# Kernel tuning notes

Hardware: AMD Instinct MI355X
Metric: run time of the kernel (lower is better)

Reference implementation:

```python
import jax, jax.numpy as jnp
import numpy as np

NUM_SRC1, NUM_DST1 = 2_000_000, 131_072
NUM_SRC2, NUM_DST2 = 131_072, 8_192
E1, E2 = NUM_DST1 * 15, NUM_DST2 * 15
F_IN, F_H = 128, 128


def setup_inputs() -> dict:
    key = jax.random.key(0)
    ks = jax.random.split(key, 10)
    return {
        "x": jax.random.normal(ks[0], (NUM_SRC1, F_IN), dtype=jnp.float32),
        "edge1_src": jax.random.randint(ks[1], (E1,), 0, NUM_SRC1, dtype=jnp.int32),
        "edge1_dst": jax.random.randint(ks[2], (E1,), 0, NUM_DST1, dtype=jnp.int32),
        "edge2_src": jax.random.randint(ks[3], (E2,), 0, NUM_SRC2, dtype=jnp.int32),
        "edge2_dst": jax.random.randint(ks[4], (E2,), 0, NUM_DST2, dtype=jnp.int32),
        "num_dst1": NUM_DST1,
        "num_dst2": NUM_DST2,
        "W_self1": jax.random.normal(ks[5], (F_IN, F_H), dtype=jnp.float32) * 0.05,
        "W_neigh1": jax.random.normal(ks[6], (F_IN, F_H), dtype=jnp.float32) * 0.05,
        "b1": jnp.zeros((F_H,), dtype=jnp.float32),
        "W_self2": jax.random.normal(ks[7], (F_H, F_H), dtype=jnp.float32) * 0.05,
        "W_neigh2": jax.random.normal(ks[8], (F_H, F_H), dtype=jnp.float32) * 0.05,
        "b2": jnp.zeros((F_H,), dtype=jnp.float32),
    }


def _sage_mean(h_src, h_dst, e_src, e_dst, num_dst, W_self, W_neigh, b):
    # mean-aggregate neighbor feats per dst, then linear transforms (DGL SAGEConv, aggr='mean')
    agg = jax.ops.segment_sum(h_src[e_src], e_dst, num_segments=num_dst)  # [num_dst, F]
    deg = jax.ops.segment_sum(jnp.ones((e_dst.shape[0],), h_src.dtype), e_dst,
                              num_segments=num_dst)
    mean = agg / jnp.maximum(deg, 1.0)[:, None]
    return h_dst @ W_self + mean @ W_neigh + b


def reference(x, edge1_src, edge1_dst, edge2_src, edge2_dst, num_dst1, num_dst2,
              W_self1, W_neigh1, b1, W_self2, W_neigh2, b2):
    h_dst = x[:num_dst1]
    h = _sage_mean(x, h_dst, edge1_src, edge1_dst, num_dst1, W_self1, W_neigh1, b1)
    h = jax.nn.relu(h)
    h_dst2 = h[:num_dst2]
    out = _sage_mean(h, h_dst2, edge2_src, edge2_dst, num_dst2, W_self2, W_neigh2, b2)
    return out
```

## Files before the change

kernel.cpp:

```cpp
#include <hip/hip_runtime.h>

static constexpr int FDIM = 128;
static constexpr int ND1  = 131072;
static constexpr int ND2  = 8192;
static constexpr int PADW = 64;
static constexpr int LDP  = 56;

using bf16x8 = __attribute__((ext_vector_type(8))) short;
using u16x8  = __attribute__((ext_vector_type(8))) unsigned short;
using f32x4  = __attribute__((ext_vector_type(4))) float;

static __device__ __forceinline__ unsigned short f2bf(float f) {
  unsigned u = __float_as_uint(f);
  u = (u + 0x7FFFu + ((u >> 16) & 1u)) >> 16;
  return (unsigned short)u;
}
static __device__ __forceinline__ float bf2f(unsigned short s) {
  return __uint_as_float(((unsigned)s) << 16);
}

__global__ void build_pad(const int* __restrict__ e1s, const int* __restrict__ e1d,
                          const int* __restrict__ e2s, const int* __restrict__ e2d,
                          int* __restrict__ cnt1, int* __restrict__ cnt2,
                          int* __restrict__ pad1, int* __restrict__ pad2,
                          int E1, int E2, int nb_fill,
                          const float* __restrict__ Ws1, const float* __restrict__ Wn1,
                          unsigned short* __restrict__ Wt1,
                          const float* __restrict__ Ws2, const float* __restrict__ Wn2,
                          unsigned short* __restrict__ Wt2) {
  if ((int)blockIdx.x >= nb_fill) {
    int t = (blockIdx.x - nb_fill) * 256 + threadIdx.x;
    int which = t >> 15;
    int r = t & 32767;
    int col = r >> 8, k = r & 255;
    const float* Ws = which ? Ws2 : Ws1;
    const float* Wn = which ? Wn2 : Wn1;
    unsigned short* Wt = which ? Wt2 : Wt1;
    float v = (k < 128) ? Ws[k * 128 + col] : Wn[(k - 128) * 128 + col];
    Wt[col * 256 + k] = f2bf(v);
    return;
  }
  const int n1 = E1 >> 2, n2 = E2 >> 2;
  int t = blockIdx.x * 256 + threadIdx.x;
  if (t < n1) {
    int4 d = ((const int4*)e1d)[t];
    int4 s = ((const int4*)e1s)[t];
    int p;
    p = atomicAdd(&cnt1[d.x], 1); if (p < PADW) pad1[d.x * PADW + p] = s.x;
    p = atomicAdd(&cnt1[d.y], 1); if (p < PADW) pad1[d.y * PADW + p] = s.y;
    p = atomicAdd(&cnt1[d.z], 1); if (p < PADW) pad1[d.z * PADW + p] = s.z;
    p = atomicAdd(&cnt1[d.w], 1); if (p < PADW) pad1[d.w * PADW + p] = s.w;
  } else if (t < n1 + n2) {
    int4 d = ((const int4*)e2d)[t - n1];
    int4 s = ((const int4*)e2s)[t - n1];
    int p;
    p = atomicAdd(&cnt2[d.x], 1); if (p < PADW) pad2[d.x * PADW + p] = s.x;
    p = atomicAdd(&cnt2[d.y], 1); if (p < PADW) pad2[d.y * PADW + p] = s.y;
    p = atomicAdd(&cnt2[d.z], 1); if (p < PADW) pad2[d.z * PADW + p] = s.z;
    p = atomicAdd(&cnt2[d.w], 1); if (p < PADW) pad2[d.w * PADW + p] = s.w;
  }
  if (blockIdx.x == 0) {
    int tt = threadIdx.x;
    if (tt < (E1 & 3)) {
      int e = E1 - 1 - tt, d = e1d[e];
      int p = atomicAdd(&cnt1[d], 1); if (p < PADW) pad1[d * PADW + p] = e1s[e];
    }
    int t2 = tt - 8;
    if (t2 >= 0 && t2 < (E2 & 3)) {
      int e = E2 - 1 - t2, d = e2d[e];
      int p = atomicAdd(&cnt2[d], 1); if (p < PADW) pad2[d * PADW + p] = e2s[e];
    }
  }
}

__global__ __launch_bounds__(256)
void gather_mean1(const float* __restrict__ src, const int* __restrict__ pad,
                  const int* __restrict__ cnt, unsigned short* __restrict__ out, int nrows) {
  const int lane = threadIdx.x & 63;
  const int half = lane >> 5;
  const int sub  = lane & 31;
  const int wid  = (int)((blockIdx.x * 256u + threadIdx.x) >> 6);
  const int row  = wid * 2 + half;
  if (row >= nrows) return;
  const int deg = cnt[row];
  float ax = 0.f, ay = 0.f, az = 0.f, aw = 0.f;
  for (int base = 0; base < deg; base += 32) {
    int t = base + sub;
    int idx = pad[row * PADW + (t < deg ? t : deg - 1)];
    const int lim = (deg - base) < 32 ? (deg - base) : 32;
    for (int b = 0; b < lim; b += 8) {
      float4 v[8];
      #pragma unroll
      for (int j = 0; j < 8; ++j) {
        int e = __shfl(idx, half * 32 + b + j);
        v[j] = *(const float4*)(src + (size_t)e * FDIM + sub * 4);
      }
      #pragma unroll
      for (int j = 0; j < 8; ++j) {
        float mk = (b + j) < lim ? 1.f : 0.f;
        ax = fmaf(v[j].x, mk, ax); ay = fmaf(v[j].y, mk, ay);
        az = fmaf(v[j].z, mk, az); aw = fmaf(v[j].w, mk, aw);
      }
    }
  }
  const float inv = 1.f / (float)(deg > 1 ? deg : 1);
  ushort4 o;
  o.x = f2bf(ax * inv); o.y = f2bf(ay * inv);
  o.z = f2bf(az * inv); o.w = f2bf(aw * inv);
  *(ushort4*)(out + (size_t)row * FDIM + sub * 4) = o;
}

__global__ __launch_bounds__(256)
void gather_mean2(const unsigned short* __restrict__ src, const int* __restrict__ pad,
                  const int* __restrict__ cnt, unsigned short* __restrict__ out, int nrows) {
  const int lane = threadIdx.x & 63;
  const int half = lane >> 5;
  const int sub  = lane & 31;
  const int wid  = (int)((blockIdx.x * 256u + threadIdx.x) >> 6);
  const int row  = wid * 2 + half;
  if (row >= nrows) return;
  const int deg = cnt[row];
  float ax = 0.f, ay = 0.f, az = 0.f, aw = 0.f;
  for (int base = 0; base < deg; base += 32) {
    int t = base + sub;
    int idx = pad[row * PADW + (t < deg ? t : deg - 1)];
    const int lim = (deg - base) < 32 ? (deg - base) : 32;
    for (int b = 0; b < lim; b += 8) {
      ushort4 v[8];
      #pragma unroll
      for (int j = 0; j < 8; ++j) {
        int e = __shfl(idx, half * 32 + b + j);
        v[j] = *(const ushort4*)(src + (size_t)e * FDIM + sub * 4);
      }
      #pragma unroll
      for (int j = 0; j < 8; ++j) {
        float mk = (b + j) < lim ? 1.f : 0.f;
        ax = fmaf(bf2f(v[j].x), mk, ax); ay = fmaf(bf2f(v[j].y), mk, ay);
        az = fmaf(bf2f(v[j].z), mk, az); aw = fmaf(bf2f(v[j].w), mk, aw);
      }
    }
  }
  const float inv = 1.f / (float)(deg > 1 ? deg : 1);
  ushort4 o;
  o.x = f2bf(ax * inv); o.y = f2bf(ay * inv);
  o.z = f2bf(az * inv); o.w = f2bf(aw * inv);
  *(ushort4*)(out + (size_t)row * FDIM + sub * 4) = o;
}

template<bool RELU, bool AX_BF16, bool OUT_F32>
__global__ __launch_bounds__(256)
void gemm_mfma(const void* __restrict__ Axp,
               const unsigned short* __restrict__ Am,
               const unsigned short* __restrict__ Wt,
               const float* __restrict__ bias,
               void* __restrict__ Outp) {
  __shared__ unsigned short Asb[128 * LDP];
  __shared__ unsigned short Wsb[128 * LDP];
  const int tid  = threadIdx.x;
  const int lane = tid & 63;
  const int w    = tid >> 6;
  const int row0 = blockIdx.x * 128;
  const int p    = lane & 15;
  const int q    = lane >> 4;

  f32x4 acc[2][8];
  #pragma unroll
  for (int m = 0; m < 2; ++m)
    #pragma unroll
    for (int n = 0; n < 8; ++n) acc[m][n] = (f32x4){0.f, 0.f, 0.f, 0.f};

  const int sr = tid >> 1;
  const int sk = (tid & 1) * 16;

  for (int c = 0; c < 8; ++c) {
    const int kc = c * 32;
    const int kl = kc & 127;
    {
      const unsigned short* wsrc = Wt + (size_t)sr * 256 + kc + sk;
      u16x8 a = *(const u16x8*)(wsrc);
      u16x8 b = *(const u16x8*)(wsrc + 8);
      *(u16x8*)&Wsb[sr * LDP + sk]     = a;
      *(u16x8*)&Wsb[sr * LDP + sk + 8] = b;
    }
    if (AX_BF16 || c >= 4) {
      const unsigned short* asrc =
          (c < 4 ? (const unsigned short*)Axp : Am) + (size_t)(row0 + sr) * FDIM + kl + sk;
      u16x8 a = *(const u16x8*)(asrc);
      u16x8 b = *(const u16x8*)(asrc + 8);
      *(u16x8*)&Asb[sr * LDP + sk]     = a;
      *(u16x8*)&Asb[sr * LDP + sk + 8] = b;
    } else {
      const float* asrc = (const float*)Axp + (size_t)(row0 + sr) * FDIM + kl + sk;
      float4 f0 = *(const float4*)(asrc);
      float4 f1 = *(const float4*)(asrc + 4);
      float4 f2 = *(const float4*)(asrc + 8);
      float4 f3 = *(const float4*)(asrc + 12);
      u16x8 a, b;
      a[0] = f2bf(f0.x); a[1] = f2bf(f0.y); a[2] = f2bf(f0.z); a[3] = f2bf(f0.w);
      a[4] = f2bf(f1.x); a[5] = f2bf(f1.y); a[6] = f2bf(f1.z); a[7] = f2bf(f1.w);
      b[0] = f2bf(f2.x); b[1] = f2bf(f2.y); b[2] = f2bf(f2.z); b[3] = f2bf(f2.w);
      b[4] = f2bf(f3.x); b[5] = f2bf(f3.y); b[6] = f2bf(f3.z); b[7] = f2bf(f3.w);
      *(u16x8*)&Asb[sr * LDP + sk]     = a;
      *(u16x8*)&Asb[sr * LDP + sk + 8] = b;
    }
    __syncthreads();
    bf16x8 af[2];
    #pragma unroll
    for (int m = 0; m < 2; ++m)
      af[m] = *(const bf16x8*)&Asb[(w * 32 + m * 16 + p) * LDP + q * 8];
    #pragma unroll
    for (int n = 0; n < 8; ++n) {
      bf16x8 bfr = *(const bf16x8*)&Wsb[(n * 16 + p) * LDP + q * 8];
      acc[0][n] = __builtin_amdgcn_mfma_f32_16x16x32_bf16(af[0], bfr, acc[0][n], 0, 0, 0);
      acc[1][n] = __builtin_amdgcn_mfma_f32_16x16x32_bf16(af[1], bfr, acc[1][n], 0, 0, 0);
    }
    __syncthreads();
  }

  #pragma unroll
  for (int n = 0; n < 8; ++n) {
    const int col = n * 16 + p;
    const float bv = bias[col];
    #pragma unroll
    for (int m = 0; m < 2; ++m) {
      #pragma unroll
      for (int r = 0; r < 4; ++r) {
        float y = acc[m][n][r] + bv;
        if (RELU) y = fmaxf(y, 0.f);
        const size_t grow = (size_t)(row0 + w * 32 + m * 16 + q * 4 + r);
        if (OUT_F32) ((float*)Outp)[grow * FDIM + col] = y;
        else         ((unsigned short*)Outp)[grow * FDIM + col] = f2bf(y);
      }
    }
  }
}

extern "C" void kernel_launch(void* const* d_in, const int* in_sizes, int n_in,
                              void* d_out, int out_size, void* d_ws, size_t ws_size,
                              hipStream_t stream) {
  const float* x   = (const float*)d_in[0];
  const int*   e1s = (const int*)d_in[1];
  const int*   e1d = (const int*)d_in[2];
  const int*   e2s = (const int*)d_in[3];
  const int*   e2d = (const int*)d_in[4];
  const float* Ws1 = (const float*)d_in[7];
  const float* Wn1 = (const float*)d_in[8];
  const float* b1  = (const float*)d_in[9];
  const float* Ws2 = (const float*)d_in[10];
  const float* Wn2 = (const float*)d_in[11];
  const float* b2  = (const float*)d_in[12];
  const int E1 = in_sizes[1];
  const int E2 = in_sizes[3];

  char* pw = (char*)d_ws;
  unsigned short* agg1 = (unsigned short*)pw; pw += (size_t)ND1 * FDIM * 2;
  unsigned short* h    = (unsigned short*)pw; pw += (size_t)ND1 * FDIM * 2;
  unsigned short* agg2 = (unsigned short*)pw; pw += (size_t)ND2 * FDIM * 2;
  unsigned short* Wt1  = (unsigned short*)pw; pw += (size_t)FDIM * 256 * 2;
  unsigned short* Wt2  = (unsigned short*)pw; pw += (size_t)FDIM * 256 * 2;
  int* pad1 = (int*)pw; pw += (size_t)ND1 * PADW * 4;
  int* pad2 = (int*)pw; pw += (size_t)ND2 * PADW * 4;
  int* cnt1 = (int*)pw; pw += (size_t)ND1 * 4;
  int* cnt2 = (int*)pw; pw += (size_t)ND2 * 4;

  hipMemsetAsync(cnt1, 0, (size_t)(ND1 + ND2) * 4, stream);

  const int n4 = (E1 >> 2) + (E2 >> 2);
  const int nb_fill = (n4 + 255) / 256;
  build_pad<<<nb_fill + 256, 256, 0, stream>>>(e1s, e1d, e2s, e2d, cnt1, cnt2,
                                               pad1, pad2, E1, E2, nb_fill,
                                               Ws1, Wn1, Wt1, Ws2, Wn2, Wt2);

  gather_mean1<<<ND1 / 8, 256, 0, stream>>>(x, pad1, cnt1, agg1, ND1);
  gemm_mfma<true, false, false><<<ND1 / 128, 256, 0, stream>>>(x, agg1, Wt1, b1, h);

  gather_mean2<<<ND2 / 8, 256, 0, stream>>>(h, pad2, cnt2, agg2, ND2);
  gemm_mfma<false, true, true><<<ND2 / 128, 256, 0, stream>>>(h, agg2, Wt2, b2, (float*)d_out);
}
```

Baseline: 419.1 us.

## Fuse neighbor mean gather into per-tile MFMA GEMM kernel via LDS

Each GEMM block now gathers and averages neighbor features for its 128 rows straight into shared memory, then runs the bf16 MFMA GEMM from there. This removes the separate gather kernels and the global write and read of the aggregated buffers. The cost is far fewer blocks and a larger LDS footprint, which lowers occupancy during the latency-bound random gather and serializes gather and GEMM within each block. Degree is also clamped to the pad width when indexing.

```diff
diff --git a/kernel.cpp b/kernel.cpp
--- a/kernel.cpp
+++ b/kernel.cpp
@@ -5,6 +5,7 @@
 static constexpr int ND2  = 8192;
 static constexpr int PADW = 64;
 static constexpr int LDP  = 56;
+static constexpr int AML  = 136;
 
 using bf16x8 = __attribute__((ext_vector_type(8))) short;
 using u16x8  = __attribute__((ext_vector_type(8))) unsigned short;
@@ -73,96 +74,74 @@
   }
 }
 
+template<bool L1>
 __global__ __launch_bounds__(256)
-void gather_mean1(const float* __restrict__ src, const int* __restrict__ pad,
-                  const int* __restrict__ cnt, unsigned short* __restrict__ out, int nrows) {
-  const int lane = threadIdx.x & 63;
-  const int half = lane >> 5;
-  const int sub  = lane & 31;
-  const int wid  = (int)((blockIdx.x * 256u + threadIdx.x) >> 6);
-  const int row  = wid * 2 + half;
-  if (row >= nrows) return;
-  const int deg = cnt[row];
-  float ax = 0.f, ay = 0.f, az = 0.f, aw = 0.f;
-  for (int base = 0; base < deg; base += 32) {
-    int t = base + sub;
-    int idx = pad[row * PADW + (t < deg ? t : deg - 1)];
-    const int lim = (deg - base) < 32 ? (deg - base) : 32;
-    for (int b = 0; b < lim; b += 8) {
-      float4 v[8];
-      #pragma unroll
-      for (int j = 0; j < 8; ++j) {
-        int e = __shfl(idx, half * 32 + b + j);
-        v[j] = *(const float4*)(src + (size_t)e * FDIM + sub * 4);
-      }
-      #pragma unroll
-      for (int j = 0; j < 8; ++j) {
-        float mk = (b + j) < lim ? 1.f : 0.f;
-        ax = fmaf(v[j].x, mk, ax); ay = fmaf(v[j].y, mk, ay);
-        az = fmaf(v[j].z, mk, az); aw = fmaf(v[j].w, mk, aw);
-      }
-    }
-  }
-  const float inv = 1.f / (float)(deg > 1 ? deg : 1);
-  ushort4 o;
-  o.x = f2bf(ax * inv); o.y = f2bf(ay * inv);
-  o.z = f2bf(az * inv); o.w = f2bf(aw * inv);
-  *(ushort4*)(out + (size_t)row * FDIM + sub * 4) = o;
-}
-
-__global__ __launch_bounds__(256)
-void gather_mean2(const unsigned short* __restrict__ src, const int* __restrict__ pad,
-                  const int* __restrict__ cnt, unsigned short* __restrict__ out, int nrows) {
-  const int lane = threadIdx.x & 63;
-  const int half = lane >> 5;
-  const int sub  = lane & 31;
-  const int wid  = (int)((blockIdx.x * 256u + threadIdx.x) >> 6);
-  const int row  = wid * 2 + half;
-  if (row >= nrows) return;
-  const int deg = cnt[row];
-  float ax = 0.f, ay = 0.f, az = 0.f, aw = 0.f;
-  for (int base = 0; base < deg; base += 32) {
-    int t = base + sub;
-    int idx = pad[row * PADW + (t < deg ? t : deg - 1)];
-    const int lim = (deg - base) < 32 ? (deg - base) : 32;
-    for (int b = 0; b < lim; b += 8) {
-      ushort4 v[8];
-      #pragma unroll
-      for (int j = 0; j < 8; ++j) {
-        int e = __shfl(idx, half * 32 + b + j);
-        v[j] = *(const ushort4*)(src + (size_t)e * FDIM + sub * 4);
-      }
-      #pragma unroll
-      for (int j = 0; j < 8; ++j) {
-        float mk = (b + j) < lim ? 1.f : 0.f;
-        ax = fmaf(bf2f(v[j].x), mk, ax); ay = fmaf(bf2f(v[j].y), mk, ay);
-        az = fmaf(bf2f(v[j].z), mk, az); aw = fmaf(bf2f(v[j].w), mk, aw);
-      }
-    }
-  }
-  const float inv = 1.f / (float)(deg > 1 ? deg : 1);
-  ushort4 o;
-  o.x = f2bf(ax * inv); o.y = f2bf(ay * inv);
-  o.z = f2bf(az * inv); o.w = f2bf(aw * inv);
-  *(ushort4*)(out + (size_t)row * FDIM + sub * 4) = o;
-}
-
-template<bool RELU, bool AX_BF16, bool OUT_F32>
-__global__ __launch_bounds__(256)
-void gemm_mfma(const void* __restrict__ Axp,
-               const unsigned short* __restrict__ Am,
-               const unsigned short* __restrict__ Wt,
-               const float* __restrict__ bias,
-               void* __restrict__ Outp) {
+void fused_layer(const void* __restrict__ selfp,
+                 const int* __restrict__ pad, const int* __restrict__ cnt,
+                 const unsigned short* __restrict__ Wt,
+                 const float* __restrict__ bias,
+                 void* __restrict__ Outp)
+{
+  __shared__ unsigned short AmL[128 * AML];
   __shared__ unsigned short Asb[128 * LDP];
   __shared__ unsigned short Wsb[128 * LDP];
   const int tid  = threadIdx.x;
   const int lane = tid & 63;
   const int w    = tid >> 6;
+  const int half = lane >> 5;
+  const int sub  = lane & 31;
   const int row0 = blockIdx.x * 128;
-  const int p    = lane & 15;
-  const int q    = lane >> 4;
-
+
+  for (int i = 0; i < 16; ++i) {
+    const int rl   = w * 32 + i * 2 + half;
+    const int row  = row0 + rl;
+    const int degt = cnt[row];
+    const int deg  = degt < PADW ? degt : PADW;
+    float ax = 0.f, ay = 0.f, az = 0.f, aw = 0.f;
+    for (int base = 0; base < deg; base += 32) {
+      int t = base + sub;
+      int idx = pad[(size_t)row * PADW + (t < deg ? t : deg - 1)];
+      const int lim = (deg - base) < 32 ? (deg - base) : 32;
+      for (int b = 0; b < lim; b += 8) {
+        if (L1) {
+          float4 v[8];
+          #pragma unroll
+          for (int j = 0; j < 8; ++j) {
+            int e = __shfl(idx, half * 32 + b + j);
+            v[j] = *(const float4*)((const float*)selfp + (size_t)e * FDIM + sub * 4);
+          }
+          #pragma unroll
+          for (int j = 0; j < 8; ++j) {
+            float mk = (b + j) < lim ? 1.f : 0.f;
+            ax = fmaf(v[j].x, mk, ax); ay = fmaf(v[j].y, mk, ay);
+            az = fmaf(v[j].z, mk, az); aw = fmaf(v[j].w, mk, aw);
+          }
+        } else {
+          ushort4 v[8];
+          #pragma unroll
+          for (int j = 0; j < 8; ++j) {
+            int e = __shfl(idx, half * 32 + b + j);
+            v[j] = *(const ushort4*)((const unsigned short*)selfp + (size_t)e * FDIM + sub * 4);
+          }
+          #pragma unroll
+          for (int j = 0; j < 8; ++j) {
+            float mk = (b + j) < lim ? 1.f : 0.f;
+            ax = fmaf(bf2f(v[j].x), mk, ax); ay = fmaf(bf2f(v[j].y), mk, ay);
+            az = fmaf(bf2f(v[j].z), mk, az); aw = fmaf(bf2f(v[j].w), mk, aw);
+          }
+        }
+      }
+    }
+    const float inv = 1.f / (float)(degt > 1 ? degt : 1);
+    ushort4 o;
+    o.x = f2bf(ax * inv); o.y = f2bf(ay * inv);
+    o.z = f2bf(az * inv); o.w = f2bf(aw * inv);
+    *(ushort4*)&AmL[rl * AML + sub * 4] = o;
+  }
+  __syncthreads();
+
+  const int p = lane & 15;
+  const int q = lane >> 4;
   f32x4 acc[2][8];
   #pragma unroll
   for (int m = 0; m < 2; ++m)
@@ -182,15 +161,20 @@
       *(u16x8*)&Wsb[sr * LDP + sk]     = a;
       *(u16x8*)&Wsb[sr * LDP + sk + 8] = b;
     }
-    if (AX_BF16 || c >= 4) {
+    if (c >= 4) {
+      u16x8 a = *(const u16x8*)&AmL[sr * AML + kl + sk];
+      u16x8 b = *(const u16x8*)&AmL[sr * AML + kl + sk + 8];
+      *(u16x8*)&Asb[sr * LDP + sk]     = a;
+      *(u16x8*)&Asb[sr * LDP + sk + 8] = b;
+    } else if (!L1) {
       const unsigned short* asrc =
-          (c < 4 ? (const unsigned short*)Axp : Am) + (size_t)(row0 + sr) * FDIM + kl + sk;
+          (const unsigned short*)selfp + (size_t)(row0 + sr) * FDIM + kl + sk;
       u16x8 a = *(const u16x8*)(asrc);
       u16x8 b = *(const u16x8*)(asrc + 8);
       *(u16x8*)&Asb[sr * LDP + sk]     = a;
       *(u16x8*)&Asb[sr * LDP + sk + 8] = b;
     } else {
-      const float* asrc = (const float*)Axp + (size_t)(row0 + sr) * FDIM + kl + sk;
+      const float* asrc = (const float*)selfp + (size_t)(row0 + sr) * FDIM + kl + sk;
       float4 f0 = *(const float4*)(asrc);
       float4 f1 = *(const float4*)(asrc + 4);
       float4 f2 = *(const float4*)(asrc + 8);
@@ -226,10 +210,10 @@
       #pragma unroll
       for (int r = 0; r < 4; ++r) {
         float y = acc[m][n][r] + bv;
-        if (RELU) y = fmaxf(y, 0.f);
+        if (L1) y = fmaxf(y, 0.f);
         const size_t grow = (size_t)(row0 + w * 32 + m * 16 + q * 4 + r);
-        if (OUT_F32) ((float*)Outp)[grow * FDIM + col] = y;
-        else         ((unsigned short*)Outp)[grow * FDIM + col] = f2bf(y);
+        if (L1) ((unsigned short*)Outp)[grow * FDIM + col] = f2bf(y);
+        else    ((float*)Outp)[grow * FDIM + col] = y;
       }
     }
   }
@@ -253,11 +237,9 @@
   const int E2 = in_sizes[3];
 
   char* pw = (char*)d_ws;
-  unsigned short* agg1 = (unsigned short*)pw; pw += (size_t)ND1 * FDIM * 2;
-  unsigned short* h    = (unsigned short*)pw; pw += (size_t)ND1 * FDIM * 2;
-  unsigned short* agg2 = (unsigned short*)pw; pw += (size_t)ND2 * FDIM * 2;
-  unsigned short* Wt1  = (unsigned short*)pw; pw += (size_t)FDIM * 256 * 2;
-  unsigned short* Wt2  = (unsigned short*)pw; pw += (size_t)FDIM * 256 * 2;
+  unsigned short* h   = (unsigned short*)pw; pw += (size_t)ND1 * FDIM * 2;
+  unsigned short* Wt1 = (unsigned short*)pw; pw += (size_t)FDIM * 256 * 2;
+  unsigned short* Wt2 = (unsigned short*)pw; pw += (size_t)FDIM * 256 * 2;
   int* pad1 = (int*)pw; pw += (size_t)ND1 * PADW * 4;
   int* pad2 = (int*)pw; pw += (size_t)ND2 * PADW * 4;
   int* cnt1 = (int*)pw; pw += (size_t)ND1 * 4;
@@ -271,9 +253,6 @@
                                                pad1, pad2, E1, E2, nb_fill,
                                                Ws1, Wn1, Wt1, Ws2, Wn2, Wt2);
 
-  gather_mean1<<<ND1 / 8, 256, 0, stream>>>(x, pad1, cnt1, agg1, ND1);
-  gemm_mfma<true, false, false><<<ND1 / 128, 256, 0, stream>>>(x, agg1, Wt1, b1, h);
-
-  gather_mean2<<<ND2 / 8, 256, 0, stream>>>(h, pad2, cnt2, agg2, ND2);
-  gemm_mfma<false, true, true><<<ND2 / 128, 256, 0, stream>>>(h, agg2, Wt2, b2, (float*)d_out);
-}
+  fused_layer<true ><<<ND1 / 128, 256, 0, stream>>>(x, pad1, cnt1, Wt1, b1, h);
+  fused_layer<false><<<ND2 / 128, 256, 0, stream>>>(h, pad2, cnt2, Wt2, b2, (float*)d_out);
+}
```

Result: slower. 442.1 us (+5.5%).
